# Optimization experiments

Hardware: AMD Instinct MI355X
Metric: run time of the kernel (lower is better)

Reference implementation:

```python
import jax, jax.numpy as jnp
import numpy as np

B, M, HWIN = 1024, 5, 25          # batch, encoder window, decoder horizon
SH, SW, HID = 64, 128, 256        # saliency map H/W, hidden size
SAL = SH * SW


def setup_inputs() -> dict:
    key = jax.random.key(0)
    ks = jax.random.split(key, 32)
    s = 0.02
    W = lambda k, shp: (jax.random.normal(k, shp, jnp.float32) * s)
    inp = {
        "enc_pos": jax.random.normal(ks[0], (B, M, 3), jnp.float32),
        "enc_sal": jax.random.uniform(ks[1], (B, M, SH, SW), jnp.float32),
        "dec_pos": jax.random.normal(ks[2], (B, 1, 3), jnp.float32),
        "dec_sal": jax.random.uniform(ks[3], (B, HWIN, SH, SW), jnp.float32),
        # fc_pos_enc / fc_sal_enc
        "Wpe": W(ks[4], (3, HID)),    "bpe": W(ks[5], (HID,)),
        "Wse": W(ks[6], (SAL, HID)),  "bse": W(ks[7], (HID,)),
        # fuse_1_enc LSTM (gate order i,f,g,o like torch)
        "Wih_e": W(ks[8], (2 * HID, 4 * HID)), "Whh_e": W(ks[9], (HID, 4 * HID)),
        "bih_e": W(ks[10], (4 * HID,)),        "bhh_e": W(ks[11], (4 * HID,)),
        # fuse_1_dec LSTM
        "Wih_d": W(ks[12], (2 * HID, 4 * HID)), "Whh_d": W(ks[13], (HID, 4 * HID)),
        "bih_d": W(ks[14], (4 * HID,)),         "bhh_d": W(ks[15], (4 * HID,)),
        # fc_pos_dec / fc_sal_dec
        "Wpd": W(ks[16], (3, HID)),   "bpd": W(ks[17], (HID,)),
        "Wsd": W(ks[18], (SAL, HID)), "bsd": W(ks[19], (HID,)),
        # fuse_2 and fc_layer_out
        "W2": W(ks[20], (HID, HID)),  "b2": W(ks[21], (HID,)),
        "Wo": W(ks[22], (HID, 3)),    "bo": W(ks[23], (3,)),
    }
    return inp


def _lstm_cell(h, c, x, Wih, Whh, b):
    g = x @ Wih + h @ Whh + b                     # [B, 4H]
    i, f, gg, o = jnp.split(g, 4, axis=-1)        # torch gate order i,f,g,o
    c = jax.nn.sigmoid(f) * c + jax.nn.sigmoid(i) * jnp.tanh(gg)
    h = jax.nn.sigmoid(o) * jnp.tanh(c)
    return h, c


def reference(enc_pos, enc_sal, dec_pos, dec_sal,
              Wpe, bpe, Wse, bse, Wih_e, Whh_e, bih_e, bhh_e,
              Wih_d, Whh_d, bih_d, bhh_d, Wpd, bpd, Wsd, bsd,
              W2, b2, Wo, bo):
    b = enc_pos.shape[0]
    hid = Whh_e.shape[0]
    # ---- encoder: per-timestep linear features, then LSTM over M steps ----
    sal_e = enc_sal.reshape(b, enc_sal.shape[1], -1) @ Wse + bse   # [B,M,H]
    pos_e = enc_pos @ Wpe + bpe                                     # [B,M,H]
    x_e = jnp.concatenate([sal_e, pos_e], axis=-1)                  # [B,M,2H]
    be = bih_e + bhh_e

    h0 = jnp.zeros((b, hid), enc_pos.dtype)
    c0 = jnp.zeros((b, hid), enc_pos.dtype)

    def enc_step(carry, xt):
        h, c = carry
        h, c = _lstm_cell(h, c, xt, Wih_e, Whh_e, be)
        return (h, c), None

    (h, c), _ = jax.lax.scan(enc_step, (h0, c0), jnp.swapaxes(x_e, 0, 1))

    sal_d = dec_sal.reshape(b, dec_sal.shape[1], -1) @ Wsd + bsd    # [B,Hw,H]
    bd = bih_d + bhh_d

    def dec_step(carry, sal_t):
        h, c, pos = carry                       # pos: [B,3]
        pf = pos @ Wpd + bpd                    # fc_pos_dec
        x = jnp.concatenate([sal_t, pf], axis=-1)
        h, c = _lstm_cell(h, c, x, Wih_d, Whh_d, bd)
        delta = (h @ W2 + b2) @ Wo + bo         # fuse_2 -> fc_layer_out
        newpos = pos + delta                    # toPosition: add delta,
        newpos = newpos / jnp.linalg.norm(newpos, axis=-1, keepdims=True)
        return (h, c, newpos), newpos

    pos0 = dec_pos[:, 0, :]
    _, outs = jax.lax.scan(dec_step, (h, c, pos0), jnp.swapaxes(sal_d, 0, 1))
    return jnp.swapaxes(outs, 0, 1)             # [B, H_WINDOW, 3]
```

## Files before the change

### kernel.cpp

```cpp
#include <hip/hip_runtime.h>

typedef _Float16 f16;
typedef _Float16 f16x4 __attribute__((ext_vector_type(4)));
typedef _Float16 f16x8 __attribute__((ext_vector_type(8)));
typedef float    f32x4 __attribute__((ext_vector_type(4)));
typedef int      i32x4 __attribute__((ext_vector_type(4)));
typedef unsigned int u32;

#define MFMA16(a,b,c) __builtin_amdgcn_mfma_f32_16x16x32_f16((a),(b),(c),0,0,0)
#define MFMAI8(a,b,c) __builtin_amdgcn_mfma_i32_16x16x64_i8((a),(b),(c),0,0,0)

typedef __attribute__((address_space(1))) const u32 gu32;
typedef __attribute__((address_space(3))) u32 lu32;

static __device__ __forceinline__ float frcp(float x){ float r; asm("v_rcp_f32 %0, %1" : "=v"(r) : "v"(x)); return r; }
static __device__ __forceinline__ float frsq(float x){ float r; asm("v_rsq_f32 %0, %1" : "=v"(r) : "v"(x)); return r; }
static __device__ __forceinline__ float sigm(float x){ return frcp(1.0f + __expf(-x)); }
static __device__ __forceinline__ float tanh_(float x){ return 1.0f - 2.0f*frcp(1.0f + __expf(2.0f*x)); }

static __device__ __forceinline__ void bar_lgkm(){
  asm volatile("s_waitcnt lgkmcnt(0)" ::: "memory");
  __builtin_amdgcn_s_barrier();
  asm volatile("" ::: "memory");
}
static __device__ __forceinline__ void bar_plain(){
  asm volatile("" ::: "memory");
  __builtin_amdgcn_s_barrier();
  asm volatile("" ::: "memory");
}

static constexpr size_t OFF_WSE_P  = 0;
static constexpr size_t OFF_WSD_P  = OFF_WSE_P  + (size_t)8192*256*2;
static constexpr size_t OFF_WIHE_P = OFF_WSD_P  + (size_t)8192*256*2;
static constexpr size_t OFF_WIHD_P = OFF_WIHE_P + (size_t)256*1024*2;
static constexpr size_t OFF_WHHE_P = OFF_WIHD_P + (size_t)256*1024*2;
static constexpr size_t OFF_WHHD_P = OFF_WHHE_P + (size_t)256*1024;
static constexpr size_t OFF_W3E    = OFF_WHHD_P + (size_t)256*1024;
static constexpr size_t OFF_W3D    = OFF_W3E   + (size_t)3*1024*4;
static constexpr size_t OFF_W2WO   = OFF_W3D   + (size_t)3*1024*4;
static constexpr size_t OFF_BIASE  = OFF_W2WO  + (size_t)256*3*4;
static constexpr size_t OFF_BIASD  = OFF_BIASE + (size_t)1024*4;
static constexpr size_t OFF_B2WO   = OFF_BIASD + (size_t)1024*4;
static constexpr size_t OFF_PREGE  = OFF_B2WO  + 256;
static constexpr size_t OFF_PREGD  = OFF_PREGE + (size_t)5120*1024*2;
static constexpr size_t OFF_END    = OFF_PREGD + (size_t)25600*1024*2;

__global__ __launch_bounds__(256) void k_prep(
    const float* __restrict__ Wse, const float* __restrict__ Wsd,
    const float* __restrict__ Wih_e, const float* __restrict__ Wih_d,
    const float* __restrict__ Whh_e, const float* __restrict__ Whh_d,
    f16* pWse, f16* pWsd, f16* pWih_e, f16* pWih_d,
    signed char* pWhh_e, signed char* pWhh_d,
    const float* __restrict__ Wpe, const float* __restrict__ bpe,
    const float* __restrict__ bih_e, const float* __restrict__ bhh_e,
    const float* __restrict__ Wpd, const float* __restrict__ bpd,
    const float* __restrict__ bih_d, const float* __restrict__ bhh_d,
    const float* __restrict__ W2, const float* __restrict__ b2,
    const float* __restrict__ Wo, const float* __restrict__ bo,
    float* W3e, float* W3d, float* biasE, float* biasD, float* W2Wo, float* b2Wo)
{
  int blk = blockIdx.x;
  if (blk < 2304) {
    const float* W; f16* o; int N, base;
    if      (blk < 1024) { W=Wse;   o=pWse;   N=256;  base=0; }
    else if (blk < 2048) { W=Wsd;   o=pWsd;   N=256;  base=1024; }
    else if (blk < 2176) { W=Wih_e; o=pWih_e; N=1024; base=2048; }
    else                 { W=Wih_d; o=pWih_d; N=1024; base=2176; }
    int tid = (blk - base)*256 + threadIdx.x;
    int l = tid & 63;
    int nct = N >> 4;
    int ctg = (tid >> 6) % nct;
    int kfg = (tid >> 6) / nct;
    int k0  = kfg*32 + ((l>>4)<<3);
    int col = ctg*16 + (l&15);
    f16x8 v;
#pragma unroll
    for (int i=0;i<8;++i) v[i] = (f16)W[(size_t)(k0+i)*N + col];
    *(f16x8*)(o + (size_t)tid*8) = v;
    return;
  }
  if (blk < 2432) {
    const float* W; signed char* o; int base;
    if (blk < 2368) { W=Whh_e; o=pWhh_e; base=2304; }
    else            { W=Whh_d; o=pWhh_d; base=2368; }
    int tid = (blk - base)*256 + threadIdx.x;
    int l = tid & 63;
    int unit = tid >> 6;
    int kfg = unit >> 6, ctg = unit & 63;
    int k0  = kfg*64 + ((l>>4)<<4);
    int col = ctg*16 + (l&15);
    signed char* dst = o + ((size_t)unit*64 + l)*16;
#pragma unroll
    for (int e=0;e<16;++e) {
      int q = __float2int_rn(W[(size_t)(k0+e)*1024 + col] * 1024.0f);
      q = q > 127 ? 127 : (q < -127 ? -127 : q);
      dst[e] = (signed char)q;
    }
    return;
  }
  int bid = blk - 2432, tid = threadIdx.x;
  if (bid < 4) {
    int j = bid*256 + tid;
    float s0=0,s1=0,s2=0,sb=0;
    for (int m=0;m<256;++m) {
      float wv = Wih_e[(size_t)(256+m)*1024 + j];
      s0 += Wpe[m]*wv; s1 += Wpe[256+m]*wv; s2 += Wpe[512+m]*wv; sb += bpe[m]*wv;
    }
    W3e[j]=s0; W3e[1024+j]=s1; W3e[2048+j]=s2;
    biasE[j] = bih_e[j] + bhh_e[j] + sb;
  } else if (bid < 8) {
    int j = (bid-4)*256 + tid;
    float s0=0,s1=0,s2=0,sb=0;
    for (int m=0;m<256;++m) {
      float wv = Wih_d[(size_t)(256+m)*1024 + j];
      s0 += Wpd[m]*wv; s1 += Wpd[256+m]*wv; s2 += Wpd[512+m]*wv; sb += bpd[m]*wv;
    }
    W3d[j]=s0; W3d[1024+j]=s1; W3d[2048+j]=s2;
    biasD[j] = bih_d[j] + bhh_d[j] + sb;
  } else if (bid == 8) {
    int c = tid;
    float s0=0,s1=0,s2=0;
    for (int m=0;m<256;++m) {
      float wv = W2[(size_t)c*256+m];
      s0 += wv*Wo[m*3+0]; s1 += wv*Wo[m*3+1]; s2 += wv*Wo[m*3+2];
    }
    W2Wo[c*3+0]=s0; W2Wo[c*3+1]=s1; W2Wo[c*3+2]=s2;
  } else {
    if (tid < 192) {
      int j = tid >> 6, lane = tid & 63;
      float s = 0.f;
      for (int m=lane;m<256;m+=64) s += b2[m]*Wo[m*3+j];
#pragma unroll
      for (int msk=1;msk<64;msk<<=1) s += __shfl_xor(s, msk);
      if (lane==0) b2Wo[j] = s + bo[j];
    }
  }
}

__global__ __launch_bounds__(256) void k_gemm_fused(
    const float* __restrict__ A0, const f16* __restrict__ W0,
    const float* __restrict__ bs0, const f16* __restrict__ Wih0,
    const float* __restrict__ bias0, f16* __restrict__ P0, int nb0, int T0,
    const float* __restrict__ pos0, const float* __restrict__ W3f0,
    const float* __restrict__ A1, const f16* __restrict__ W1,
    const float* __restrict__ bs1, const f16* __restrict__ Wih1,
    const float* __restrict__ bias1, f16* __restrict__ P1, int T1)
{
  __shared__ f16 aLDS[2][64*64];
  __shared__ f16 sLDS[64*256];
  const int tid = threadIdx.x, l = tid & 63, w = tid >> 6;
  const int li = l & 15, hi = l >> 4;
  const int bx = blockIdx.x;
  const float *Ap, *bs, *bias, *posf, *W3f; const f16 *Wp, *Wih; f16* P; int rblk, T;
  if (bx < nb0) { Ap=A0; Wp=W0; bs=bs0; Wih=Wih0; bias=bias0; P=P0; rblk=bx*64;       T=T0; posf=pos0; W3f=W3f0; }
  else          { Ap=A1; Wp=W1; bs=bs1; Wih=Wih1; bias=bias1; P=P1; rblk=(bx-nb0)*64; T=T1; posf=nullptr; W3f=nullptr; }
  const int t = rblk >> 10, b0 = rblk & 1023;

  f32x4 acc[4][4];
#pragma unroll
  for (int a=0;a<4;++a)
#pragma unroll
    for (int b=0;b<4;++b) acc[a][b] = (f32x4){0.f,0.f,0.f,0.f};

  const int srow = tid >> 2, kseg = tid & 3;
  const float* Arow = Ap + ((size_t)(b0 + srow)*T + t)*8192 + kseg*16;

  float4 fA0,fA1,fA2,fA3, fB0,fB1,fB2,fB3;
#define LOADA_A(ti_) { const float* Aq = Arow + (ti_)*64;                      \
    fA0 = *(const float4*)Aq;     fA1 = *(const float4*)(Aq+4);                \
    fA2 = *(const float4*)(Aq+8); fA3 = *(const float4*)(Aq+12); }
#define LOADA_B(ti_) { const float* Aq = Arow + (ti_)*64;                      \
    fB0 = *(const float4*)Aq;     fB1 = *(const float4*)(Aq+4);                \
    fB2 = *(const float4*)(Aq+8); fB3 = *(const float4*)(Aq+12); }
#define MFMA_TILE(buf_, kfg0_)                                                 \
  _Pragma("unroll")                                                            \
  for (int kf = 0; kf < 2; ++kf) {                                             \
    f16x8 afr[4], bfr[4];                                                      \
    _Pragma("unroll")                                                          \
    for (int rt=0; rt<4; ++rt) {                                               \
      int row = rt*16 + li;                                                    \
      afr[rt] = *(f16x8*)&aLDS[buf_][row*64 + (((kf*4) + hi) ^ (row&7))*8];    \
    }                                                                          \
    _Pragma("unroll")                                                          \
    for (int ct=0; ct<4; ++ct) {                                               \
      int ctg = w*4 + ct;                                                      \
      bfr[ct] = *(const f16x8*)(Wp + ((size_t)(((kfg0_)+kf)*16 + ctg)*64 + l)*8); \
    }                                                                          \
    _Pragma("unroll")                                                          \
    for (int rt=0; rt<4; ++rt)                                                 \
      _Pragma("unroll")                                                        \
      for (int ct=0; ct<4; ++ct)                                               \
        acc[rt][ct] = MFMA16(afr[rt], bfr[ct], acc[rt][ct]);                   \
  }
#define STAGE1_STEP(F0,F1,F2,F3, RELOAD, buf_, ti_) {                          \
    f16x8 w0, w1;               \
    w0[0]=(f16)F0.x; w0[1]=(f16)F0.y; w0[2]=(f16)F0.z; w0[3]=(f16)F0.w;        \
    w0[4]=(f16)F1.x; w0[5]=(f16)F1.y; w0[6]=(f16)F1.z; w0[7]=(f16)F1.w;        \
    w1[0]=(f16)F2.x; w1[1]=(f16)F2.y; w1[2]=(f16)F2.z; w1[3]=(f16)F2.w;        \
    w1[4]=(f16)F3.x; w1[5]=(f16)F3.y; w1[6]=(f16)F3.z; w1[7]=(f16)F3.w;        \
    bar_plain();                     \
    *(f16x8*)&aLDS[buf_][srow*64 + ((kseg*2    ) ^ (srow&7))*8] = w0;          \
    *(f16x8*)&aLDS[buf_][srow*64 + ((kseg*2 + 1) ^ (srow&7))*8] = w1;          \
    { int tn = ((ti_)+2 < 128) ? (ti_)+2 : 127; RELOAD(tn); }                  \
    bar_lgkm();                       \
    MFMA_TILE(buf_, (ti_)*2)                                                   \
  }

  LOADA_A(0); LOADA_B(1);
  for (int ti = 0; ti < 128; ti += 2) {
    STAGE1_STEP(fA0,fA1,fA2,fA3, LOADA_A, 0, ti)
    STAGE1_STEP(fB0,fB1,fB2,fB3, LOADA_B, 1, ti+1)
  }
#undef LOADA_A
#undef LOADA_B
#undef MFMA_TILE
#undef STAGE1_STEP
  bar_plain();
#pragma unroll
  for (int ct=0; ct<4; ++ct) {
    int col = (w*4 + ct)*16 + li;
    float bv = bs[col];
    int slot = col >> 3;
#pragma unroll
    for (int rt=0; rt<4; ++rt)
#pragma unroll
      for (int i=0;i<4;++i) {
        int row = rt*16 + hi*4 + i;
        sLDS[row*256 + ((slot ^ (row&7))<<3) + (col&7)] = (f16)(acc[rt][ct][i] + bv);
      }
  }
  float pe[4][4][3];
  if (posf) {
#pragma unroll
    for (int rt=0; rt<4; ++rt)
#pragma unroll
      for (int i=0;i<4;++i) {
        int brow = b0 + rt*16 + hi*4 + i;
        const float* pq = posf + ((size_t)brow*T + t)*3;
        pe[rt][i][0]=pq[0]; pe[rt][i][1]=pq[1]; pe[rt][i][2]=pq[2];
      }
  }
  __syncthreads();
  const int bblk0 = b0 >> 4;
#pragma unroll
  for (int cg=0; cg<4; ++cg) {
    f32x4 a2[4][4];
#pragma unroll
    for (int a=0;a<4;++a)
#pragma unroll
      for (int b=0;b<4;++b) a2[a][b] = (f32x4){0.f,0.f,0.f,0.f};
#pragma unroll
    for (int kfg=0; kfg<8; ++kfg) {
      f16x8 afr[4], bfr[4];
#pragma unroll
      for (int rt=0; rt<4; ++rt) {
        int row = rt*16 + li;
        afr[rt] = *(f16x8*)&sLDS[row*256 + (((kfg*4 + hi) ^ (row&7))<<3)];
      }
#pragma unroll
      for (int ct=0; ct<4; ++ct) {
        int ctg2 = cg*16 + w*4 + ct;
        bfr[ct] = *(const f16x8*)(Wih + ((size_t)(kfg*64 + ctg2)*64 + l)*8);
      }
#pragma unroll
      for (int rt=0; rt<4; ++rt)
#pragma unroll
        for (int ct=0; ct<4; ++ct)
          a2[rt][ct] = MFMA16(afr[rt], bfr[ct], a2[rt][ct]);
    }
#pragma unroll
    for (int ct=0; ct<4; ++ct) {
      const int ctg2 = cg*16 + w*4 + ct;
      const float bv = bias[ctg2*16 + li];
      float w30=0.f, w31=0.f, w32=0.f;
      if (posf) { int gc = ctg2*16 + li; w30=W3f[gc]; w31=W3f[1024+gc]; w32=W3f[2048+gc]; }
#pragma unroll
      for (int rt=0; rt<4; ++rt) {
        f16x4 o;
#pragma unroll
        for (int i=0;i<4;++i) {
          float v = a2[rt][ct][i] + bv;
          if (posf) v += pe[rt][i][0]*w30 + pe[rt][i][1]*w31 + pe[rt][i][2]*w32;
          o[i] = (f16)v;
        }
        *(f16x4*)(P + ((size_t)((bblk0 + rt)*T + t)*64 + ctg2)*256 + l*4) = o;
      }
    }
  }
}

__global__ __launch_bounds__(512) void k_rnn(
    const f16* __restrict__ pregE,
    const f16* __restrict__ pregD,
    const signed char* __restrict__ Whh_e_p, const signed char* __restrict__ Whh_d_p,
    const float* __restrict__ W3d, const float* __restrict__ dec_pos,
    const float* __restrict__ W2Wo, const float* __restrict__ b2Wo,
    float* __restrict__ out)
{
  __shared__ signed char wLDS[8][4][4][1024];
  __shared__ signed char hBuf[2][16*256];
  __shared__ f16 W3h[3*1024];
  __shared__ float dpart[25][16][3];
  const int tid = threadIdx.x, l = tid & 63, w = tid >> 6;
  const int li = l & 15, hi = l >> 4;
  const int bblk = blockIdx.x, rb = bblk*16;
  const float SC = 1.0f/130048.0f;

  for (int i=tid;i<3072;i+=512) W3h[i] = (f16)W3d[i];
  for (int i=tid; i<25*16*3; i+=512) ((float*)dpart)[i] = 0.f;

  float c_st[2][4];
#pragma unroll
  for (int j=0;j<2;++j)
#pragma unroll
    for (int i=0;i<4;++i) c_st[j][i]=0.f;

#define VMW(n) { asm volatile("s_waitcnt vmcnt(" #n ")" ::: "memory");        \
                 __builtin_amdgcn_sched_barrier(0); }
#define STAGE(WP, kf, h, s)                                                   \
  _Pragma("unroll") for (int f=0; f<4; ++f) {                                 \
    int ctg = ((h)*2 + (f>>1))*16 + w*2 + (f&1);                              \
    const signed char* g = (WP) + ((size_t)((kf)*64 + ctg)*64 + l)*16;        \
    __builtin_amdgcn_global_load_lds((gu32*)g, (lu32*)&wLDS[w][s][f][0], 16, 0, 0); \
  }
#define AH(ah, hB, kf) ah = *(i32x4*)&(hB)[li*256 + ((((kf)*4)+hi) ^ (li&7))*16];
#define MFMA4(s, h, ah)                                                       \
  _Pragma("unroll") for (int f=0; f<4; ++f) {                                 \
    i32x4 b = *(i32x4*)&wLDS[w][s][f][l*16];                                  \
    acc[(h)*2 + (f>>1)][f&1] = MFMAI8(ah, b, acc[(h)*2 + (f>>1)][f&1]); }
#define KFSTREAM8(hB, WP, WPn, PVB, PVT) {                                    \
  i32x4 ah;                                                                   \
  VMW(8) AH(ah, hB, 0) MFMA4(0, 0, ah) STAGE(WP, 1, 1, 3)                     \
  VMW(8)               MFMA4(1, 1, ah) STAGE(WP, 2, 0, 0)                     \
  VMW(8) AH(ah, hB, 1) MFMA4(2, 0, ah) STAGE(WP, 2, 1, 1)                     \
  VMW(8)               MFMA4(3, 1, ah) STAGE(WP, 3, 0, 2)                     \
  VMW(8) AH(ah, hB, 2) MFMA4(0, 0, ah) STAGE(WP, 3, 1, 3)                     \
  VMW(8)               MFMA4(1, 1, ah) LOADPV(pvB, PVB, PVT) STAGE(WPn, 0, 0, 0) \
  VMW(24) AH(ah, hB, 3) MFMA4(2, 0, ah) STAGE(WPn, 0, 1, 1)                   \
  VMW(24)               MFMA4(3, 1, ah) STAGE(WPn, 1, 0, 2)                   \
  }
#define LOADPV(dst, base, t_)                                                 \
  _Pragma("unroll")                                                           \
  for (int q=0;q<4;++q)                                                       \
    _Pragma("unroll")                                                         \
    for (int j=0;j<2;++j)                                                     \
      dst[q][j] = *(const f16x4*)((base) + ((size_t)(t_)*16384 + (size_t)(q*16 + w*2 + j)*256 + l*4));
#define COPYPV()                                                              \
  _Pragma("unroll")                                                           \
  for (int q=0;q<4;++q)                                                       \
    _Pragma("unroll")                                                         \
    for (int j=0;j<2;++j) pvA[q][j] = pvB[q][j];
#define ACCZERO()                                                             \
  i32x4 acc[4][2];                                                            \
  _Pragma("unroll")                                                           \
  for (int q=0;q<4;++q)                                                       \
    _Pragma("unroll")                                                         \
    for (int j=0;j<2;++j) acc[q][j] = (i32x4){0,0,0,0};
#define HWRITE(hB, r, hc, hval)                                               \
  (hB)[(r)*256 + ((((hc)>>4) ^ ((r)&7))<<4) + ((hc)&15)] =                    \
      (signed char)__float2int_rn((hval)*127.0f);

  const f16* prE = pregE + (size_t)bblk*5*16384;
  const f16* prD = pregD + (size_t)bblk*25*16384;
  f16x4 pvA[4][2], pvB[4][2];

  __syncthreads();
  LOADPV(pvA, prE, 0)
  STAGE(Whh_e_p,0,0,0) STAGE(Whh_e_p,0,1,1) STAGE(Whh_e_p,1,0,2)

  for (int t=0;t<5;++t) {
    ACCZERO()
    if (t > 0) {
      if (t < 4) { KFSTREAM8(hBuf[(t-1)&1], Whh_e_p, Whh_e_p, prE, t+1) }
      else       { KFSTREAM8(hBuf[(t-1)&1], Whh_e_p, Whh_d_p, prD, 0)   }
    }
#pragma unroll
    for (int i=0;i<4;++i) {
      int r = hi*4 + i;
#pragma unroll
      for (int j=0;j<2;++j) {
        int hc = w*32 + j*16 + li;
        float gq[4];
#pragma unroll
        for (int q=0;q<4;++q)
          gq[q] = (float)pvA[q][j][i] + (float)acc[q][j][i]*SC;
        float cn = sigm(gq[1])*c_st[j][i] + sigm(gq[0])*tanh_(gq[2]);
        c_st[j][i] = cn;
        float h = sigm(gq[3])*tanh_(cn);
        HWRITE(hBuf[t&1], r, hc, h)
      }
    }
    if (t == 0) LOADPV(pvB, prE, 1)
    COPYPV()
    bar_lgkm();
  }

  float w2r[2][3];
#pragma unroll
  for (int j=0;j<2;++j) {
    int hc = w*32 + j*16 + li;
    w2r[j][0]=W2Wo[hc*3+0]; w2r[j][1]=W2Wo[hc*3+1]; w2r[j][2]=W2Wo[hc*3+2];
  }
  const float b2w0 = b2Wo[0], b2w1 = b2Wo[1], b2w2 = b2Wo[2];
  float pp[4][3];
#pragma unroll
  for (int i=0;i<4;++i) {
    int r = rb + hi*4 + i;
    pp[i][0]=dec_pos[r*3+0]; pp[i][1]=dec_pos[r*3+1]; pp[i][2]=dec_pos[r*3+2];
  }

  for (int t=0;t<25;++t) {
    ACCZERO()
    if (t+1 < 25) { KFSTREAM8(hBuf[t&1], Whh_d_p, Whh_d_p, prD, t+1) }
    else          { KFSTREAM8(hBuf[t&1], Whh_d_p, Whh_d_p, prD, 24)  }
    float w3v[2][4][3];
#pragma unroll
    for (int j=0;j<2;++j)
#pragma unroll
      for (int q=0;q<4;++q) {
        int gc = q*256 + w*32 + j*16 + li;
        w3v[j][q][0] = (float)W3h[gc];
        w3v[j][q][1] = (float)W3h[1024+gc];
        w3v[j][q][2] = (float)W3h[2048+gc];
      }
    float dpar[4][3];
#pragma unroll
    for (int i=0;i<4;++i){ dpar[i][0]=0.f; dpar[i][1]=0.f; dpar[i][2]=0.f; }
#pragma unroll
    for (int i=0;i<4;++i) {
      int r = hi*4 + i;
#pragma unroll
      for (int j=0;j<2;++j) {
        int hc = w*32 + j*16 + li;
        float gq[4];
#pragma unroll
        for (int q=0;q<4;++q)
          gq[q] = (float)pvA[q][j][i] + (float)acc[q][j][i]*SC
                + pp[i][0]*w3v[j][q][0] + pp[i][1]*w3v[j][q][1] + pp[i][2]*w3v[j][q][2];
        float cn = sigm(gq[1])*c_st[j][i] + sigm(gq[0])*tanh_(gq[2]);
        c_st[j][i] = cn;
        float h = sigm(gq[3])*tanh_(cn);
        HWRITE(hBuf[(t+1)&1], r, hc, h)
        dpar[i][0] += h*w2r[j][0];
        dpar[i][1] += h*w2r[j][1];
        dpar[i][2] += h*w2r[j][2];
      }
    }
#pragma unroll
    for (int m=1;m<16;m<<=1)
#pragma unroll
      for (int i=0;i<4;++i) {
        dpar[i][0] += __shfl_xor(dpar[i][0], m);
        dpar[i][1] += __shfl_xor(dpar[i][1], m);
        dpar[i][2] += __shfl_xor(dpar[i][2], m);
      }
    if (li==0) {
#pragma unroll
      for (int i=0;i<4;++i) {
        int r = hi*4 + i;
        atomicAdd(&dpart[t][r][0], dpar[i][0]);
        atomicAdd(&dpart[t][r][1], dpar[i][1]);
        atomicAdd(&dpart[t][r][2], dpar[i][2]);
      }
    }
    COPYPV()
    bar_lgkm();
#pragma unroll
    for (int i=0;i<4;++i) {
      int r = hi*4 + i;
      float p0 = pp[i][0] + b2w0 + dpart[t][r][0];
      float p1 = pp[i][1] + b2w1 + dpart[t][r][1];
      float p2 = pp[i][2] + b2w2 + dpart[t][r][2];
      float inv = frsq(p0*p0+p1*p1+p2*p2);
      pp[i][0]=p0*inv; pp[i][1]=p1*inv; pp[i][2]=p2*inv;
      if (w==0 && li==0) {
        float* o = out + (size_t)(rb+r)*75 + t*3;
        o[0]=pp[i][0]; o[1]=pp[i][1]; o[2]=pp[i][2];
      }
    }
  }
#undef VMW
#undef STAGE
#undef AH
#undef MFMA4
#undef KFSTREAM8
#undef LOADPV
#undef COPYPV
#undef ACCZERO
#undef HWRITE
}

extern "C" void kernel_launch(void* const* d_in, const int* in_sizes, int n_in,
                              void* d_out, int out_size, void* d_ws, size_t ws_size,
                              hipStream_t stream)
{
  const float* enc_pos = (const float*)d_in[0];
  const float* enc_sal = (const float*)d_in[1];
  const float* dec_pos = (const float*)d_in[2];
  const float* dec_sal = (const float*)d_in[3];
  const float* Wpe  = (const float*)d_in[4];
  const float* bpe  = (const float*)d_in[5];
  const float* Wse  = (const float*)d_in[6];
  const float* bse  = (const float*)d_in[7];
  const float* Wih_e= (const float*)d_in[8];
  const float* Whh_e= (const float*)d_in[9];
  const float* bih_e= (const float*)d_in[10];
  const float* bhh_e= (const float*)d_in[11];
  const float* Wih_d= (const float*)d_in[12];
  const float* Whh_d= (const float*)d_in[13];
  const float* bih_d= (const float*)d_in[14];
  const float* bhh_d= (const float*)d_in[15];
  const float* Wpd  = (const float*)d_in[16];
  const float* bpd  = (const float*)d_in[17];
  const float* Wsd  = (const float*)d_in[18];
  const float* bsd  = (const float*)d_in[19];
  const float* W2   = (const float*)d_in[20];
  const float* b2   = (const float*)d_in[21];
  const float* Wo   = (const float*)d_in[22];
  const float* bo   = (const float*)d_in[23];

  char* ws = (char*)d_ws;
  f16* pWse   = (f16*)(ws + OFF_WSE_P);
  f16* pWsd   = (f16*)(ws + OFF_WSD_P);
  f16* pWih_e = (f16*)(ws + OFF_WIHE_P);
  f16* pWih_d = (f16*)(ws + OFF_WIHD_P);
  signed char* pWhh_e = (signed char*)(ws + OFF_WHHE_P);
  signed char* pWhh_d = (signed char*)(ws + OFF_WHHD_P);
  float* W3e  = (float*)(ws + OFF_W3E);
  float* W3d  = (float*)(ws + OFF_W3D);
  float* W2WoP= (float*)(ws + OFF_W2WO);
  float* biasE= (float*)(ws + OFF_BIASE);
  float* biasD= (float*)(ws + OFF_BIASD);
  float* b2WoP= (float*)(ws + OFF_B2WO);
  f16* pregE  = (f16*)(ws + OFF_PREGE);
  f16* pregD  = (f16*)(ws + OFF_PREGD);
  float* out  = (float*)d_out;

  hipLaunchKernelGGL(k_prep, dim3(2442), dim3(256), 0, stream,
                     Wse, Wsd, Wih_e, Wih_d, Whh_e, Whh_d,
                     pWse, pWsd, pWih_e, pWih_d, pWhh_e, pWhh_d,
                     Wpe, bpe, bih_e, bhh_e, Wpd, bpd, bih_d, bhh_d,
                     W2, b2, Wo, bo,
                     W3e, W3d, biasE, biasD, W2WoP, b2WoP);
  hipLaunchKernelGGL(k_gemm_fused, dim3(480), dim3(256), 0, stream,
                     enc_sal, pWse, bse, pWih_e, biasE, pregE, 80, 5, enc_pos, W3e,
                     dec_sal, pWsd, bsd, pWih_d, biasD, pregD, 25);
  hipLaunchKernelGGL(k_rnn, dim3(64), dim3(512), 0, stream,
                     pregE, pregD, pWhh_e, pWhh_d,
                     W3d, dec_pos, W2WoP, b2WoP, out);
}
```

Measured before the change: 505.5 us.

## Fuse GEMM and RNN kernels with per-tile flags to overlap recurrence with projection

Merges the saliency-projection GEMM kernel and the LSTM recurrence kernel into a single persistent launch. Blocks 0-63 run the recurrence and spin on per-(timestep, batch-group) flags, while the remaining 240 blocks compute 128-row GEMM tiles and publish completion with release stores. The GEMM tile is also doubled to 128 rows with 512 threads per block. The aim is to hide the recurrence latency behind the GEMM and remove one kernel launch boundary. The risks are spin-wait overhead, deadlock if the recurrence blocks occupy CUs needed by the GEMM blocks, and changed occupancy from the larger shared-memory footprint.

```diff
diff --git a/kernel.cpp b/kernel.cpp
--- a/kernel.cpp
+++ b/kernel.cpp
@@ -27,6 +27,12 @@
   asm volatile("" ::: "memory");
   __builtin_amdgcn_s_barrier();
   asm volatile("" ::: "memory");
+}
+static __device__ __forceinline__ void waitflag(u32* f){
+  if (__hip_atomic_load(f, __ATOMIC_ACQUIRE, __HIP_MEMORY_SCOPE_AGENT)) return;
+  while (__hip_atomic_load(f, __ATOMIC_RELAXED, __HIP_MEMORY_SCOPE_AGENT) == 0)
+    __builtin_amdgcn_s_sleep(8);
+  (void)__hip_atomic_load(f, __ATOMIC_ACQUIRE, __HIP_MEMORY_SCOPE_AGENT);
 }
 
 static constexpr size_t OFF_WSE_P  = 0;
@@ -43,7 +49,7 @@
 static constexpr size_t OFF_B2WO   = OFF_BIASD + (size_t)1024*4;
 static constexpr size_t OFF_PREGE  = OFF_B2WO  + 256;
 static constexpr size_t OFF_PREGD  = OFF_PREGE + (size_t)5120*1024*2;
-static constexpr size_t OFF_END    = OFF_PREGD + (size_t)25600*1024*2;
+static constexpr size_t OFF_FLAGS  = OFF_PREGD + (size_t)25600*1024*2;
 
 __global__ __launch_bounds__(256) void k_prep(
     const float* __restrict__ Wse, const float* __restrict__ Wsd,
@@ -57,7 +63,8 @@
     const float* __restrict__ bih_d, const float* __restrict__ bhh_d,
     const float* __restrict__ W2, const float* __restrict__ b2,
     const float* __restrict__ Wo, const float* __restrict__ bo,
-    float* W3e, float* W3d, float* biasE, float* biasD, float* W2Wo, float* b2Wo)
+    float* W3e, float* W3d, float* biasE, float* biasD, float* W2Wo, float* b2Wo,
+    u32* flags)
 {
   int blk = blockIdx.x;
   if (blk < 2304) {
@@ -125,7 +132,7 @@
       s0 += wv*Wo[m*3+0]; s1 += wv*Wo[m*3+1]; s2 += wv*Wo[m*3+2];
     }
     W2Wo[c*3+0]=s0; W2Wo[c*3+1]=s1; W2Wo[c*3+2]=s2;
-  } else {
+  } else if (bid == 9) {
     if (tid < 192) {
       int j = tid >> 6, lane = tid & 63;
       float s = 0.f;
@@ -134,176 +141,180 @@
       for (int msk=1;msk<64;msk<<=1) s += __shfl_xor(s, msk);
       if (lane==0) b2Wo[j] = s + bo[j];
     }
+  } else {
+    if (tid < 240) flags[tid] = 0u;
   }
 }
 
-__global__ __launch_bounds__(256) void k_gemm_fused(
+__global__ __launch_bounds__(512) void k_main(
     const float* __restrict__ A0, const f16* __restrict__ W0,
     const float* __restrict__ bs0, const f16* __restrict__ Wih0,
-    const float* __restrict__ bias0, f16* __restrict__ P0, int nb0, int T0,
+    const float* __restrict__ bias0, f16* __restrict__ P0,
     const float* __restrict__ pos0, const float* __restrict__ W3f0,
     const float* __restrict__ A1, const f16* __restrict__ W1,
     const float* __restrict__ bs1, const f16* __restrict__ Wih1,
-    const float* __restrict__ bias1, f16* __restrict__ P1, int T1)
+    const float* __restrict__ bias1, f16* __restrict__ P1,
+    const signed char* __restrict__ Whh_e_p, const signed char* __restrict__ Whh_d_p,
+    const float* __restrict__ W3d, const float* __restrict__ dec_pos,
+    const float* __restrict__ W2Wo, const float* __restrict__ b2Wo,
+    u32* flags, float* __restrict__ out)
 {
-  __shared__ f16 aLDS[2][64*64];
-  __shared__ f16 sLDS[64*256];
+  __shared__ __align__(16) char smem[150208];
   const int tid = threadIdx.x, l = tid & 63, w = tid >> 6;
   const int li = l & 15, hi = l >> 4;
   const int bx = blockIdx.x;
-  const float *Ap, *bs, *bias, *posf, *W3f; const f16 *Wp, *Wih; f16* P; int rblk, T;
-  if (bx < nb0) { Ap=A0; Wp=W0; bs=bs0; Wih=Wih0; bias=bias0; P=P0; rblk=bx*64;       T=T0; posf=pos0; W3f=W3f0; }
-  else          { Ap=A1; Wp=W1; bs=bs1; Wih=Wih1; bias=bias1; P=P1; rblk=(bx-nb0)*64; T=T1; posf=nullptr; W3f=nullptr; }
-  const int t = rblk >> 10, b0 = rblk & 1023;
-
-  f32x4 acc[4][4];
-#pragma unroll
-  for (int a=0;a<4;++a)
-#pragma unroll
-    for (int b=0;b<4;++b) acc[a][b] = (f32x4){0.f,0.f,0.f,0.f};
-
-  const int srow = tid >> 2, kseg = tid & 3;
-  const float* Arow = Ap + ((size_t)(b0 + srow)*T + t)*8192 + kseg*16;
-
-  float4 fA0,fA1,fA2,fA3, fB0,fB1,fB2,fB3;
+
+  if (bx >= 64) {
+    f16 (*aLDS)[8192] = (f16(*)[8192])smem;
+    f16* sLDS = (f16*)(smem + 32768);
+    const int wr = w >> 2, wc = w & 3;
+    const int gx = bx - 64;
+    const float *Ap,*bs,*bias,*posf,*W3f; const f16 *Wp,*Wih; f16* P; int t,b0,T;
+    if (gx < 40) { t=gx>>3; b0=(gx&7)<<7; Ap=A0;Wp=W0;bs=bs0;Wih=Wih0;bias=bias0;P=P0;T=5; posf=pos0; W3f=W3f0; }
+    else { int d=gx-40; t=d>>3; b0=(d&7)<<7; Ap=A1;Wp=W1;bs=bs1;Wih=Wih1;bias=bias1;P=P1;T=25; posf=nullptr; W3f=nullptr; }
+
+    f32x4 acc[4][4];
+#pragma unroll
+    for (int a=0;a<4;++a)
+#pragma unroll
+      for (int b=0;b<4;++b) acc[a][b] = (f32x4){0.f,0.f,0.f,0.f};
+
+    const int arow = tid >> 2, kseg = tid & 3;
+    const float* Arow = Ap + ((size_t)(b0 + arow)*T + t)*8192 + kseg*16;
+
+    float4 fA0,fA1,fA2,fA3, fB0,fB1,fB2,fB3;
 #define LOADA_A(ti_) { const float* Aq = Arow + (ti_)*64;                      \
     fA0 = *(const float4*)Aq;     fA1 = *(const float4*)(Aq+4);                \
     fA2 = *(const float4*)(Aq+8); fA3 = *(const float4*)(Aq+12); }
 #define LOADA_B(ti_) { const float* Aq = Arow + (ti_)*64;                      \
     fB0 = *(const float4*)Aq;     fB1 = *(const float4*)(Aq+4);                \
     fB2 = *(const float4*)(Aq+8); fB3 = *(const float4*)(Aq+12); }
-#define MFMA_TILE(buf_, kfg0_)                                                 \
-  _Pragma("unroll")                                                            \
-  for (int kf = 0; kf < 2; ++kf) {                                             \
-    f16x8 afr[4], bfr[4];                                                      \
+#define GMFMA(buf_, kfg0_)                                                     \
     _Pragma("unroll")                                                          \
-    for (int rt=0; rt<4; ++rt) {                                               \
-      int row = rt*16 + li;                                                    \
-      afr[rt] = *(f16x8*)&aLDS[buf_][row*64 + (((kf*4) + hi) ^ (row&7))*8];    \
-    }                                                                          \
-    _Pragma("unroll")                                                          \
-    for (int ct=0; ct<4; ++ct) {                                               \
-      int ctg = w*4 + ct;                                                      \
-      bfr[ct] = *(const f16x8*)(Wp + ((size_t)(((kfg0_)+kf)*16 + ctg)*64 + l)*8); \
-    }                                                                          \
-    _Pragma("unroll")                                                          \
-    for (int rt=0; rt<4; ++rt)                                                 \
+    for (int kf = 0; kf < 2; ++kf) {                                           \
+      f16x8 afr[4], bfr[4];                                                    \
       _Pragma("unroll")                                                        \
-      for (int ct=0; ct<4; ++ct)                                               \
-        acc[rt][ct] = MFMA16(afr[rt], bfr[ct], acc[rt][ct]);                   \
-  }
-#define STAGE1_STEP(F0,F1,F2,F3, RELOAD, buf_, ti_) {                          \
-    f16x8 w0, w1;               \
-    w0[0]=(f16)F0.x; w0[1]=(f16)F0.y; w0[2]=(f16)F0.z; w0[3]=(f16)F0.w;        \
-    w0[4]=(f16)F1.x; w0[5]=(f16)F1.y; w0[6]=(f16)F1.z; w0[7]=(f16)F1.w;        \
-    w1[0]=(f16)F2.x; w1[1]=(f16)F2.y; w1[2]=(f16)F2.z; w1[3]=(f16)F2.w;        \
-    w1[4]=(f16)F3.x; w1[5]=(f16)F3.y; w1[6]=(f16)F3.z; w1[7]=(f16)F3.w;        \
-    bar_plain();                     \
-    *(f16x8*)&aLDS[buf_][srow*64 + ((kseg*2    ) ^ (srow&7))*8] = w0;          \
-    *(f16x8*)&aLDS[buf_][srow*64 + ((kseg*2 + 1) ^ (srow&7))*8] = w1;          \
-    { int tn = ((ti_)+2 < 128) ? (ti_)+2 : 127; RELOAD(tn); }                  \
-    bar_lgkm();                       \
-    MFMA_TILE(buf_, (ti_)*2)                                                   \
-  }
-
-  LOADA_A(0); LOADA_B(1);
-  for (int ti = 0; ti < 128; ti += 2) {
-    STAGE1_STEP(fA0,fA1,fA2,fA3, LOADA_A, 0, ti)
-    STAGE1_STEP(fB0,fB1,fB2,fB3, LOADA_B, 1, ti+1)
-  }
+      for (int rt=0; rt<4; ++rt) {                                             \
+        int row = wr*64 + rt*16 + li;                                          \
+        afr[rt] = *(f16x8*)&aLDS[buf_][row*64 + (((kf*4) + hi) ^ (row&7))*8];  \
+      }                                                                        \
+      _Pragma("unroll")                                                        \
+      for (int ct=0; ct<4; ++ct) {                                             \
+        int ctg = wc*4 + ct;                                                   \
+        bfr[ct] = *(const f16x8*)(Wp + ((size_t)(((kfg0_)+kf)*16 + ctg)*64 + l)*8); \
+      }                                                                        \
+      _Pragma("unroll")                                                        \
+      for (int rt=0; rt<4; ++rt)                                               \
+        _Pragma("unroll")                                                      \
+        for (int ct=0; ct<4; ++ct)                                             \
+          acc[rt][ct] = MFMA16(afr[rt], bfr[ct], acc[rt][ct]);                 \
+    }
+#define GSTEP(F0,F1,F2,F3, RELOAD, buf_, ti_) {                                \
+      f16x8 w0, w1;                                                            \
+      w0[0]=(f16)F0.x; w0[1]=(f16)F0.y; w0[2]=(f16)F0.z; w0[3]=(f16)F0.w;      \
+      w0[4]=(f16)F1.x; w0[5]=(f16)F1.y; w0[6]=(f16)F1.z; w0[7]=(f16)F1.w;      \
+      w1[0]=(f16)F2.x; w1[1]=(f16)F2.y; w1[2]=(f16)F2.z; w1[3]=(f16)F2.w;      \
+      w1[4]=(f16)F3.x; w1[5]=(f16)F3.y; w1[6]=(f16)F3.z; w1[7]=(f16)F3.w;      \
+      bar_plain();                                                             \
+      *(f16x8*)&aLDS[buf_][arow*64 + ((kseg*2    ) ^ (arow&7))*8] = w0;        \
+      *(f16x8*)&aLDS[buf_][arow*64 + ((kseg*2 + 1) ^ (arow&7))*8] = w1;        \
+      { int tn = ((ti_)+2 < 128) ? (ti_)+2 : 127; RELOAD(tn); }                \
+      bar_lgkm();                                                              \
+      GMFMA(buf_, (ti_)*2)                                                     \
+    }
+
+    LOADA_A(0); LOADA_B(1);
+    for (int ti = 0; ti < 128; ti += 2) {
+      GSTEP(fA0,fA1,fA2,fA3, LOADA_A, 0, ti)
+      GSTEP(fB0,fB1,fB2,fB3, LOADA_B, 1, ti+1)
+    }
 #undef LOADA_A
 #undef LOADA_B
-#undef MFMA_TILE
-#undef STAGE1_STEP
-  bar_plain();
-#pragma unroll
-  for (int ct=0; ct<4; ++ct) {
-    int col = (w*4 + ct)*16 + li;
-    float bv = bs[col];
-    int slot = col >> 3;
-#pragma unroll
-    for (int rt=0; rt<4; ++rt)
-#pragma unroll
-      for (int i=0;i<4;++i) {
-        int row = rt*16 + hi*4 + i;
-        sLDS[row*256 + ((slot ^ (row&7))<<3) + (col&7)] = (f16)(acc[rt][ct][i] + bv);
-      }
-  }
-  float pe[4][4][3];
-  if (posf) {
-#pragma unroll
-    for (int rt=0; rt<4; ++rt)
-#pragma unroll
-      for (int i=0;i<4;++i) {
-        int brow = b0 + rt*16 + hi*4 + i;
-        const float* pq = posf + ((size_t)brow*T + t)*3;
-        pe[rt][i][0]=pq[0]; pe[rt][i][1]=pq[1]; pe[rt][i][2]=pq[2];
-      }
-  }
-  __syncthreads();
-  const int bblk0 = b0 >> 4;
-#pragma unroll
-  for (int cg=0; cg<4; ++cg) {
-    f32x4 a2[4][4];
-#pragma unroll
-    for (int a=0;a<4;++a)
-#pragma unroll
-      for (int b=0;b<4;++b) a2[a][b] = (f32x4){0.f,0.f,0.f,0.f};
-#pragma unroll
-    for (int kfg=0; kfg<8; ++kfg) {
-      f16x8 afr[4], bfr[4];
-#pragma unroll
-      for (int rt=0; rt<4; ++rt) {
-        int row = rt*16 + li;
-        afr[rt] = *(f16x8*)&sLDS[row*256 + (((kfg*4 + hi) ^ (row&7))<<3)];
+#undef GMFMA
+#undef GSTEP
+    bar_plain();
+#pragma unroll
+    for (int ct=0; ct<4; ++ct) {
+      int col = (wc*4 + ct)*16 + li;
+      float bv = bs[col];
+      int slot = col >> 3;
+#pragma unroll
+      for (int rt=0; rt<4; ++rt)
+#pragma unroll
+        for (int i=0;i<4;++i) {
+          int row = wr*64 + rt*16 + hi*4 + i;
+          sLDS[row*256 + ((slot ^ (row&7))<<3) + (col&7)] = (f16)(acc[rt][ct][i] + bv);
+        }
+    }
+    float pe[4][4][3];
+    if (posf) {
+#pragma unroll
+      for (int rt=0; rt<4; ++rt)
+#pragma unroll
+        for (int i=0;i<4;++i) {
+          int brow = b0 + wr*64 + rt*16 + hi*4 + i;
+          const float* pq = posf + ((size_t)brow*T + t)*3;
+          pe[rt][i][0]=pq[0]; pe[rt][i][1]=pq[1]; pe[rt][i][2]=pq[2];
+        }
+    }
+    __syncthreads();
+#pragma unroll
+    for (int cg=0; cg<4; ++cg) {
+      f32x4 a2[4][4];
+#pragma unroll
+      for (int a=0;a<4;++a)
+#pragma unroll
+        for (int b=0;b<4;++b) a2[a][b] = (f32x4){0.f,0.f,0.f,0.f};
+#pragma unroll
+      for (int kfg=0; kfg<8; ++kfg) {
+        f16x8 afr[4], bfr[4];
+#pragma unroll
+        for (int rt=0; rt<4; ++rt) {
+          int row = wr*64 + rt*16 + li;
+          afr[rt] = *(f16x8*)&sLDS[row*256 + (((kfg*4 + hi) ^ (row&7))<<3)];
+        }
+#pragma unroll
+        for (int ct=0; ct<4; ++ct) {
+          int ctg2 = cg*16 + wc*4 + ct;
+          bfr[ct] = *(const f16x8*)(Wih + ((size_t)(kfg*64 + ctg2)*64 + l)*8);
+        }
+#pragma unroll
+        for (int rt=0; rt<4; ++rt)
+#pragma unroll
+          for (int ct=0; ct<4; ++ct)
+            a2[rt][ct] = MFMA16(afr[rt], bfr[ct], a2[rt][ct]);
       }
 #pragma unroll
       for (int ct=0; ct<4; ++ct) {
-        int ctg2 = cg*16 + w*4 + ct;
-        bfr[ct] = *(const f16x8*)(Wih + ((size_t)(kfg*64 + ctg2)*64 + l)*8);
-      }
-#pragma unroll
-      for (int rt=0; rt<4; ++rt)
-#pragma unroll
-        for (int ct=0; ct<4; ++ct)
-          a2[rt][ct] = MFMA16(afr[rt], bfr[ct], a2[rt][ct]);
-    }
-#pragma unroll
-    for (int ct=0; ct<4; ++ct) {
-      const int ctg2 = cg*16 + w*4 + ct;
-      const float bv = bias[ctg2*16 + li];
-      float w30=0.f, w31=0.f, w32=0.f;
-      if (posf) { int gc = ctg2*16 + li; w30=W3f[gc]; w31=W3f[1024+gc]; w32=W3f[2048+gc]; }
-#pragma unroll
-      for (int rt=0; rt<4; ++rt) {
-        f16x4 o;
-#pragma unroll
-        for (int i=0;i<4;++i) {
-          float v = a2[rt][ct][i] + bv;
-          if (posf) v += pe[rt][i][0]*w30 + pe[rt][i][1]*w31 + pe[rt][i][2]*w32;
-          o[i] = (f16)v;
+        const int ctg2 = cg*16 + wc*4 + ct;
+        const float bv = bias[ctg2*16 + li];
+        float w30=0.f, w31=0.f, w32=0.f;
+        if (posf) { int gc = ctg2*16 + li; w30=W3f[gc]; w31=W3f[1024+gc]; w32=W3f[2048+gc]; }
+#pragma unroll
+        for (int rt=0; rt<4; ++rt) {
+          f16x4 o;
+#pragma unroll
+          for (int i=0;i<4;++i) {
+            float v = a2[rt][ct][i] + bv;
+            if (posf) v += pe[rt][i][0]*w30 + pe[rt][i][1]*w31 + pe[rt][i][2]*w32;
+            o[i] = (f16)v;
+          }
+          int bb = (b0>>4) + wr*4 + rt;
+          *(f16x4*)(P + ((size_t)(bb*T + t)*64 + ctg2)*256 + l*4) = o;
         }
-        *(f16x4*)(P + ((size_t)((bblk0 + rt)*T + t)*64 + ctg2)*256 + l*4) = o;
-      }
-    }
-  }
-}
-
-__global__ __launch_bounds__(512) void k_rnn(
-    const f16* __restrict__ pregE,
-    const f16* __restrict__ pregD,
-    const signed char* __restrict__ Whh_e_p, const signed char* __restrict__ Whh_d_p,
-    const float* __restrict__ W3d, const float* __restrict__ dec_pos,
-    const float* __restrict__ W2Wo, const float* __restrict__ b2Wo,
-    float* __restrict__ out)
-{
-  __shared__ signed char wLDS[8][4][4][1024];
-  __shared__ signed char hBuf[2][16*256];
-  __shared__ f16 W3h[3*1024];
-  __shared__ float dpart[25][16][3];
-  const int tid = threadIdx.x, l = tid & 63, w = tid >> 6;
-  const int li = l & 15, hi = l >> 4;
-  const int bblk = blockIdx.x, rb = bblk*16;
+      }
+    }
+    __syncthreads();
+    if (tid == 0)
+      __hip_atomic_store(&flags[gx], 1u, __ATOMIC_RELEASE, __HIP_MEMORY_SCOPE_AGENT);
+    return;
+  }
+
+  signed char (*wLDS)[4][4][1024] = (signed char(*)[4][4][1024])smem;
+  signed char (*hBuf)[16*256] = (signed char(*)[16*256])(smem + 131072);
+  f16* W3h = (f16*)(smem + 139264);
+  float (*dpart)[16][3] = (float(*)[16][3])(smem + 145408);
+  const int bblk = bx, rb = bblk*16, g = bblk >> 3;
   const float SC = 1.0f/130048.0f;
 
   for (int i=tid;i<3072;i+=512) W3h[i] = (f16)W3d[i];
@@ -320,8 +331,8 @@
 #define STAGE(WP, kf, h, s)                                                   \
   _Pragma("unroll") for (int f=0; f<4; ++f) {                                 \
     int ctg = ((h)*2 + (f>>1))*16 + w*2 + (f&1);                              \
-    const signed char* g = (WP) + ((size_t)((kf)*64 + ctg)*64 + l)*16;        \
-    __builtin_amdgcn_global_load_lds((gu32*)g, (lu32*)&wLDS[w][s][f][0], 16, 0, 0); \
+    const signed char* gp = (WP) + ((size_t)((kf)*64 + ctg)*64 + l)*16;       \
+    __builtin_amdgcn_global_load_lds((gu32*)gp, (lu32*)&wLDS[w][s][f][0], 16, 0, 0); \
   }
 #define AH(ah, hB, kf) ah = *(i32x4*)&(hB)[li*256 + ((((kf)*4)+hi) ^ (li&7))*16];
 #define MFMA4(s, h, ah)                                                       \
@@ -336,8 +347,8 @@
   VMW(8)               MFMA4(3, 1, ah) STAGE(WP, 3, 0, 2)                     \
   VMW(8) AH(ah, hB, 2) MFMA4(0, 0, ah) STAGE(WP, 3, 1, 3)                     \
   VMW(8)               MFMA4(1, 1, ah) LOADPV(pvB, PVB, PVT) STAGE(WPn, 0, 0, 0) \
-  VMW(24) AH(ah, hB, 3) MFMA4(2, 0, ah) STAGE(WPn, 0, 1, 1)                   \
-  VMW(24)               MFMA4(3, 1, ah) STAGE(WPn, 1, 0, 2)                   \
+  VMW(16) AH(ah, hB, 3) MFMA4(2, 0, ah) STAGE(WPn, 0, 1, 1)                   \
+  VMW(16)               MFMA4(3, 1, ah) STAGE(WPn, 1, 0, 2)                   \
   }
 #define LOADPV(dst, base, t_)                                                 \
   _Pragma("unroll")                                                           \
@@ -360,15 +371,18 @@
   (hB)[(r)*256 + ((((hc)>>4) ^ ((r)&7))<<4) + ((hc)&15)] =                    \
       (signed char)__float2int_rn((hval)*127.0f);
 
-  const f16* prE = pregE + (size_t)bblk*5*16384;
-  const f16* prD = pregD + (size_t)bblk*25*16384;
+  const f16* prE = P0 + (size_t)bblk*5*16384;
+  const f16* prD = P1 + (size_t)bblk*25*16384;
   f16x4 pvA[4][2], pvB[4][2];
 
   __syncthreads();
+  STAGE(Whh_e_p,0,0,0) STAGE(Whh_e_p,0,1,1) STAGE(Whh_e_p,1,0,2)
+  waitflag(&flags[0*8 + g]);
   LOADPV(pvA, prE, 0)
-  STAGE(Whh_e_p,0,0,0) STAGE(Whh_e_p,0,1,1) STAGE(Whh_e_p,1,0,2)
 
   for (int t=0;t<5;++t) {
+    if (t < 4) waitflag(&flags[(t+1)*8 + g]);
+    else       waitflag(&flags[40 + 0*8 + g]);
     ACCZERO()
     if (t > 0) {
       if (t < 4) { KFSTREAM8(hBuf[(t-1)&1], Whh_e_p, Whh_e_p, prE, t+1) }
@@ -410,6 +424,7 @@
   }
 
   for (int t=0;t<25;++t) {
+    if (t+1 < 25) waitflag(&flags[40 + (t+1)*8 + g]);
     ACCZERO()
     if (t+1 < 25) { KFSTREAM8(hBuf[t&1], Whh_d_p, Whh_d_p, prD, t+1) }
     else          { KFSTREAM8(hBuf[t&1], Whh_d_p, Whh_d_p, prD, 24)  }
@@ -534,18 +549,18 @@
   float* b2WoP= (float*)(ws + OFF_B2WO);
   f16* pregE  = (f16*)(ws + OFF_PREGE);
   f16* pregD  = (f16*)(ws + OFF_PREGD);
+  u32* flags  = (u32*)(ws + OFF_FLAGS);
   float* out  = (float*)d_out;
 
-  hipLaunchKernelGGL(k_prep, dim3(2442), dim3(256), 0, stream,
+  hipLaunchKernelGGL(k_prep, dim3(2443), dim3(256), 0, stream,
                      Wse, Wsd, Wih_e, Wih_d, Whh_e, Whh_d,
                      pWse, pWsd, pWih_e, pWih_d, pWhh_e, pWhh_d,
                      Wpe, bpe, bih_e, bhh_e, Wpd, bpd, bih_d, bhh_d,
                      W2, b2, Wo, bo,
-                     W3e, W3d, biasE, biasD, W2WoP, b2WoP);
-  hipLaunchKernelGGL(k_gemm_fused, dim3(480), dim3(256), 0, stream,
-                     enc_sal, pWse, bse, pWih_e, biasE, pregE, 80, 5, enc_pos, W3e,
-                     dec_sal, pWsd, bsd, pWih_d, biasD, pregD, 25);
-  hipLaunchKernelGGL(k_rnn, dim3(64), dim3(512), 0, stream,
-                     pregE, pregD, pWhh_e, pWhh_d,
-                     W3d, dec_pos, W2WoP, b2WoP, out);
+                     W3e, W3d, biasE, biasD, W2WoP, b2WoP, flags);
+  hipLaunchKernelGGL(k_main, dim3(304), dim3(512), 0, stream,
+                     enc_sal, pWse, bse, pWih_e, biasE, pregE, enc_pos, W3e,
+                     dec_sal, pWsd, bsd, pWih_d, biasD, pregD,
+                     pWhh_e, pWhh_d, W3d, dec_pos, W2WoP, b2WoP,
+                     flags, out);
 }
```

After: 756.8 us. +49.7%, slower.
